# Kernel optimization log

Measured on AMD Instinct MI355X. Metric: run time of the kernel, lower is better.

The kernel has to match this reference:

```python
import jax, jax.numpy as jnp
import numpy as np
import math

EMBED_DIM = 1024
NUM_HEADS = 16
HEAD_DIM = EMBED_DIM // NUM_HEADS
TGT_LEN = 1024
BSZ = 4


def setup_inputs() -> dict:
    key = jax.random.key(0)
    ks = jax.random.split(key, 7)
    # xavier_uniform for in_proj_weight [3E, E]
    limit = math.sqrt(6.0 / (3 * EMBED_DIM + EMBED_DIM))
    in_proj_weight = jax.random.uniform(ks[0], (3 * EMBED_DIM, EMBED_DIM), jnp.float32, -limit, limit)
    in_proj_bias = jnp.zeros((3 * EMBED_DIM,), jnp.float32)
    # out_proj: torch Linear default init (kaiming-uniform-ish); bias zeroed by _reset_parameters
    lim_o = 1.0 / math.sqrt(EMBED_DIM)
    out_proj_weight = jax.random.uniform(ks[1], (EMBED_DIM, EMBED_DIM), jnp.float32, -lim_o, lim_o)
    out_proj_bias = jnp.zeros((EMBED_DIM,), jnp.float32)
    query = jax.random.normal(ks[2], (TGT_LEN, BSZ, EMBED_DIM), jnp.float32)
    key_t = jax.random.normal(ks[3], (TGT_LEN, BSZ, EMBED_DIM), jnp.float32)
    value = jax.random.normal(ks[4], (TGT_LEN, BSZ, EMBED_DIM), jnp.float32)
    return {"query": query, "key": key_t, "value": value,
            "in_proj_weight": in_proj_weight, "in_proj_bias": in_proj_bias,
            "out_proj_weight": out_proj_weight, "out_proj_bias": out_proj_bias}


def reference(query, key, value, in_proj_weight, in_proj_bias, out_proj_weight, out_proj_bias):
    tgt_len, bsz, embed_dim = query.shape
    src_len = key.shape[0]
    w_q, w_k, w_v = jnp.split(in_proj_weight, 3, axis=0)
    b_q, b_k, b_v = jnp.split(in_proj_bias, 3, axis=0)
    q = query @ w_q.T + b_q  # [T, B, E]
    k = key @ w_k.T + b_k    # [S, B, E]
    v = value @ w_v.T + b_v  # [S, B, E]
    # [T, B*H, D] -> [B*H, T, D]
    q = q.reshape(tgt_len, bsz * NUM_HEADS, HEAD_DIM).transpose(1, 0, 2)
    k = k.reshape(src_len, bsz * NUM_HEADS, HEAD_DIM).transpose(1, 0, 2)
    v = v.reshape(src_len, bsz * NUM_HEADS, HEAD_DIM).transpose(1, 0, 2)
    q = q / math.sqrt(embed_dim)  # NOTE: scales by sqrt(embed_dim), not head_dim (faithful)
    attn = jax.nn.sigmoid(jnp.einsum('btd,bsd->bts', q, k))  # [B*H, T, S]
    attn_output = jnp.einsum('bts,bsd->btd', attn, v)         # [B*H, T, D]
    attn_output = attn_output.transpose(1, 0, 2).reshape(tgt_len, bsz, embed_dim)
    attn_output = attn_output @ out_proj_weight.T + out_proj_bias
    return attn_output, attn
```

## Files before the change

kernel.cpp:

```cpp
#include <hip/hip_runtime.h>
#include <stdint.h>

typedef unsigned short u16;
typedef __bf16 bf16x8 __attribute__((ext_vector_type(8)));
typedef float f32x4 __attribute__((ext_vector_type(4)));

__device__ __forceinline__ u16 f2bf(float f) {
  union { float f; uint32_t u; } v; v.f = f;
  uint32_t u = v.u;
  return (u16)((u + 0x7FFFu + ((u >> 16) & 1u)) >> 16);
}

__device__ __forceinline__ void cp16(const void* g, void* lds) {
  __builtin_amdgcn_global_load_lds(
      (const __attribute__((address_space(1))) uint32_t*)(uintptr_t)g,
      (__attribute__((address_space(3))) uint32_t*)(uint32_t)(uintptr_t)lds,
      16, 0, 0);
}

__global__ __launch_bounds__(256) void cvt_kernel(const float* __restrict__ s,
                                                  u16* __restrict__ d, int n4) {
  int i = blockIdx.x * 256 + threadIdx.x;
  if (i >= n4) return;
  float4 f = ((const float4*)s)[i];
  uint2 p;
  p.x = (uint32_t)f2bf(f.x) | ((uint32_t)f2bf(f.y) << 16);
  p.y = (uint32_t)f2bf(f.z) | ((uint32_t)f2bf(f.w) << 16);
  ((uint2*)d)[i] = p;
}

__device__ __forceinline__ void gemm128(const u16* __restrict__ A,
                                        const u16* __restrict__ Bt,
                                        int m0, int n0, int K,
                                        u16* As, u16* Bs, f32x4 acc[4][4]) {
  const int tid = threadIdx.x;
  const int l = tid & 63, w = tid >> 6;
  const int wr = w >> 1, wc = w & 1;
  const int quad = l >> 4, c = l & 15;
  const f32x4 zero = {0.f, 0.f, 0.f, 0.f};
  for (int i = 0; i < 4; ++i)
    for (int j = 0; j < 4; ++j) acc[i][j] = zero;

  for (int k0 = 0; k0 < K; k0 += 64) {
    __syncthreads();
#pragma unroll
    for (int p = 0; p < 4; ++p) {
      int q = p * 256 + tid;
      int row = q >> 3;
      int jj = (q & 7) ^ (row & 7);
      int ldsbase = (p * 256 + (tid & ~63)) * 8;
      cp16(A + (size_t)(m0 + row) * K + k0 + jj * 8, As + ldsbase);
      cp16(Bt + (size_t)(n0 + row) * K + k0 + jj * 8, Bs + ldsbase);
    }
    __syncthreads();
#pragma unroll
    for (int kk = 0; kk < 2; ++kk) {
      bf16x8 af[4], bf[4];
#pragma unroll
      for (int mt = 0; mt < 4; ++mt) {
        int row = wr * 64 + mt * 16 + c;
        af[mt] = *(const bf16x8*)(As + row * 64 + ((((kk << 2) + quad)) ^ (c & 7)) * 8);
      }
#pragma unroll
      for (int nt = 0; nt < 4; ++nt) {
        int row = wc * 64 + nt * 16 + c;
        bf[nt] = *(const bf16x8*)(Bs + row * 64 + ((((kk << 2) + quad)) ^ (c & 7)) * 8);
      }
#pragma unroll
      for (int mt = 0; mt < 4; ++mt)
#pragma unroll
        for (int nt = 0; nt < 4; ++nt)
          acc[mt][nt] = __builtin_amdgcn_mfma_f32_16x16x32_bf16(
              af[mt], bf[nt], acc[mt][nt], 0, 0, 0);
    }
  }
}

__global__ __launch_bounds__(256, 2) void proj_kernel(
    const u16* __restrict__ X, const u16* __restrict__ Win,
    const float* __restrict__ in_bias, u16* __restrict__ Q,
    u16* __restrict__ Kp, u16* __restrict__ Vtmp) {
  __shared__ u16 As[8192], Bs[8192];
  const int which = blockIdx.z;
  const u16* A = X + (size_t)which * (4096 * 1024);
  const u16* Bt = Win + (size_t)which * (1024 * 1024);
  const int m0 = blockIdx.y * 128, n0 = blockIdx.x * 128;
  f32x4 acc[4][4];
  gemm128(A, Bt, m0, n0, 1024, As, Bs, acc);

  u16* dst = (which == 0) ? Q : ((which == 1) ? Kp : Vtmp);
  const float scale = (which == 0) ? 0.03125f : 1.0f;
  const float* bias = in_bias + which * 1024;
  const int l = threadIdx.x & 63, w = threadIdx.x >> 6;
  const int wr = w >> 1, wc = w & 1, quad = l >> 4, c = l & 15;
#pragma unroll
  for (int mt = 0; mt < 4; ++mt)
#pragma unroll
    for (int nt = 0; nt < 4; ++nt) {
      int n = n0 + wc * 64 + nt * 16 + c;
      float bv = bias[n];
      int h = n >> 6, d = n & 63;
#pragma unroll
      for (int r = 0; r < 4; ++r) {
        int m = m0 + wr * 64 + mt * 16 + quad * 4 + r;
        int t = m >> 2, b = m & 3;
        dst[((size_t)((b * 16 + h) * 1024 + t)) * 64 + d] =
            f2bf((acc[mt][nt][r] + bv) * scale);
      }
    }
}

__global__ __launch_bounds__(256, 2) void outproj_kernel(
    const u16* __restrict__ AO, const u16* __restrict__ Wout,
    const float* __restrict__ out_bias, float* __restrict__ out) {
  __shared__ u16 As[8192], Bs[8192];
  const int m0 = blockIdx.y * 128, n0 = blockIdx.x * 128;
  f32x4 acc[4][4];
  gemm128(AO, Wout, m0, n0, 1024, As, Bs, acc);
  const int l = threadIdx.x & 63, w = threadIdx.x >> 6;
  const int wr = w >> 1, wc = w & 1, quad = l >> 4, c = l & 15;
#pragma unroll
  for (int mt = 0; mt < 4; ++mt)
#pragma unroll
    for (int nt = 0; nt < 4; ++nt) {
      int n = n0 + wc * 64 + nt * 16 + c;
      float bv = out_bias[n];
#pragma unroll
      for (int r = 0; r < 4; ++r) {
        int m = m0 + wr * 64 + mt * 16 + quad * 4 + r;
        out[(size_t)m * 1024 + n] = acc[mt][nt][r] + bv;
      }
    }
}

__global__ __launch_bounds__(256) void transpose_v(const u16* __restrict__ Vtmp,
                                                   u16* __restrict__ Vt) {
  __shared__ u16 tile[64 * 72];
  const int bh = blockIdx.y, s0 = blockIdx.x * 64;
  const u16* src = Vtmp + (size_t)bh * 65536;
  u16* dst = Vt + (size_t)bh * 65536;
#pragma unroll
  for (int p = 0; p < 2; ++p) {
    int q = p * 256 + threadIdx.x;
    int sl = q >> 3, dc = q & 7;
    uint4 v = *(const uint4*)(src + (size_t)(s0 + sl) * 64 + dc * 8);
    *(uint4*)&tile[sl * 72 + dc * 8] = v;
  }
  __syncthreads();
#pragma unroll
  for (int p = 0; p < 2; ++p) {
    int q = p * 256 + threadIdx.x;
    int d = q >> 3, sc = q & 7;
    u16 vals[8] __attribute__((aligned(16)));
#pragma unroll
    for (int j = 0; j < 8; ++j) vals[j] = tile[(sc * 8 + j) * 72 + d];
    *(uint4*)(dst + (size_t)d * 1024 + s0 + sc * 8) = *(const uint4*)vals;
  }
}

__global__ __launch_bounds__(256, 2) void attn_kernel(
    const u16* __restrict__ Q, const u16* __restrict__ Kg,
    const u16* __restrict__ Vt, float* __restrict__ attn_out,
    u16* __restrict__ AO) {
  __shared__ u16 Qs[8192];
  __shared__ u16 U[16384];
  __shared__ u16 Vts[8192];
  const int bh = blockIdx.y, t0 = blockIdx.x * 128;
  const int b = bh >> 4, h = bh & 15;
  const int tid = threadIdx.x, l = tid & 63, w = tid >> 6;
  const int quad = l >> 4, c = l & 15;
  const int wr = w >> 1, wc = w & 1;
  const u16* Qbh = Q + (size_t)bh * 65536;
  const u16* Kbh = Kg + (size_t)bh * 65536;
  const u16* Vtbh = Vt + (size_t)bh * 65536;
  float* attnb = attn_out + (size_t)bh * 1048576;

#pragma unroll
  for (int p = 0; p < 4; ++p) {
    int q = p * 256 + tid;
    int row = q >> 3, jj = (q & 7) ^ (row & 7);
    cp16(Qbh + (size_t)(t0 + row) * 64 + jj * 8, Qs + (p * 256 + (tid & ~63)) * 8);
  }

  const f32x4 zero = {0.f, 0.f, 0.f, 0.f};
  f32x4 acc_o[2][4];
  for (int i = 0; i < 2; ++i)
    for (int j = 0; j < 4; ++j) acc_o[i][j] = zero;

  for (int s0 = 0; s0 < 1024; s0 += 128) {
    __syncthreads();
#pragma unroll
    for (int p = 0; p < 4; ++p) {
      int q = p * 256 + tid;
      int row = q >> 3, jj = (q & 7) ^ (row & 7);
      cp16(Kbh + (size_t)(s0 + row) * 64 + jj * 8, U + (p * 256 + (tid & ~63)) * 8);
    }
#pragma unroll
    for (int p = 0; p < 4; ++p) {
      int q = p * 256 + tid;
      int d = q >> 4, sc = q & 15;
      uint4 v = *(const uint4*)(Vtbh + (size_t)d * 1024 + s0 + sc * 8);
      *(uint4*)&Vts[d * 128 + (sc ^ (d & 15)) * 8] = v;
    }
    __syncthreads();

    f32x4 accp[4][4];
    for (int i = 0; i < 4; ++i)
      for (int j = 0; j < 4; ++j) accp[i][j] = zero;
#pragma unroll
    for (int kk = 0; kk < 2; ++kk) {
      bf16x8 af[4], bf[4];
#pragma unroll
      for (int mt = 0; mt < 4; ++mt) {
        int row = wr * 64 + mt * 16 + c;
        af[mt] = *(const bf16x8*)(U + row * 64 + (((kk << 2) + quad) ^ (c & 7)) * 8);
      }
#pragma unroll
      for (int nt = 0; nt < 4; ++nt) {
        int row = wc * 64 + nt * 16 + c;
        bf[nt] = *(const bf16x8*)(Qs + row * 64 + (((kk << 2) + quad) ^ (c & 7)) * 8);
      }
#pragma unroll
      for (int mt = 0; mt < 4; ++mt)
#pragma unroll
        for (int nt = 0; nt < 4; ++nt)
          accp[mt][nt] = __builtin_amdgcn_mfma_f32_16x16x32_bf16(
              af[mt], bf[nt], accp[mt][nt], 0, 0, 0);
    }

#pragma unroll
    for (int mt = 0; mt < 4; ++mt) {
      int sl = wr * 64 + mt * 16 + quad * 4;
#pragma unroll
      for (int nt = 0; nt < 4; ++nt) {
        int t = wc * 64 + nt * 16 + c;
        f32x4 pv;
#pragma unroll
        for (int r = 0; r < 4; ++r)
          pv[r] = 1.0f / (1.0f + __expf(-accp[mt][nt][r]));
        accp[mt][nt] = pv;
        *(f32x4*)(attnb + (size_t)(t0 + t) * 1024 + s0 + sl) = pv;
      }
    }
    __syncthreads();

#pragma unroll
    for (int mt = 0; mt < 4; ++mt) {
      int sbase = wr * 64 + mt * 16 + quad * 4;
      int jw = sbase >> 3, hf = (sbase >> 2) & 1;
#pragma unroll
      for (int nt = 0; nt < 4; ++nt) {
        int t = wc * 64 + nt * 16 + c;
        int jj = jw ^ (t & 15);
        uint2 pk;
        pk.x = (uint32_t)f2bf(accp[mt][nt][0]) | ((uint32_t)f2bf(accp[mt][nt][1]) << 16);
        pk.y = (uint32_t)f2bf(accp[mt][nt][2]) | ((uint32_t)f2bf(accp[mt][nt][3]) << 16);
        *(uint2*)&U[t * 128 + jj * 8 + hf * 4] = pk;
      }
    }
    __syncthreads();

#pragma unroll
    for (int kk = 0; kk < 4; ++kk) {
      bf16x8 ap[2], bv[4];
#pragma unroll
      for (int mt = 0; mt < 2; ++mt) {
        int row = w * 32 + mt * 16 + c;
        ap[mt] = *(const bf16x8*)(U + row * 128 + (((kk << 2) + quad) ^ (row & 15)) * 8);
      }
#pragma unroll
      for (int nt = 0; nt < 4; ++nt) {
        int d = nt * 16 + c;
        bv[nt] = *(const bf16x8*)(Vts + d * 128 + (((kk << 2) + quad) ^ (d & 15)) * 8);
      }
#pragma unroll
      for (int mt = 0; mt < 2; ++mt)
#pragma unroll
        for (int nt = 0; nt < 4; ++nt)
          acc_o[mt][nt] = __builtin_amdgcn_mfma_f32_16x16x32_bf16(
              ap[mt], bv[nt], acc_o[mt][nt], 0, 0, 0);
    }
  }

#pragma unroll
  for (int mt = 0; mt < 2; ++mt)
#pragma unroll
    for (int nt = 0; nt < 4; ++nt) {
      int d = nt * 16 + c;
#pragma unroll
      for (int r = 0; r < 4; ++r) {
        int t = t0 + w * 32 + mt * 16 + quad * 4 + r;
        AO[(size_t)(t * 4 + b) * 1024 + h * 64 + d] = f2bf(acc_o[mt][nt][r]);
      }
    }
}

extern "C" void kernel_launch(void* const* d_in, const int* in_sizes, int n_in,
                              void* d_out, int out_size, void* d_ws, size_t ws_size,
                              hipStream_t stream) {
  const float* query = (const float*)d_in[0];
  const float* key = (const float*)d_in[1];
  const float* value = (const float*)d_in[2];
  const float* in_w = (const float*)d_in[3];
  const float* in_b = (const float*)d_in[4];
  const float* out_w = (const float*)d_in[5];
  const float* out_b = (const float*)d_in[6];
  float* out = (float*)d_out;

  u16* ws = (u16*)d_ws;
  u16* xq = ws;
  u16* win = ws + 12582912;
  u16* wout = ws + 15728640;
  u16* Qp = ws + 16777216;
  u16* Kp = ws + 20971520;
  u16* Vt = ws + 25165824;
  u16* Vtmp = ws + 29360128;
  u16* AO = ws + 33554432;

  cvt_kernel<<<4096, 256, 0, stream>>>(query, xq, 1048576);
  cvt_kernel<<<4096, 256, 0, stream>>>(key, xq + 4194304, 1048576);
  cvt_kernel<<<4096, 256, 0, stream>>>(value, xq + 8388608, 1048576);
  cvt_kernel<<<3072, 256, 0, stream>>>(in_w, win, 786432);
  cvt_kernel<<<1024, 256, 0, stream>>>(out_w, wout, 262144);

  proj_kernel<<<dim3(8, 32, 3), 256, 0, stream>>>(xq, win, in_b, Qp, Kp, Vtmp);
  transpose_v<<<dim3(16, 64), 256, 0, stream>>>(Vtmp, Vt);
  attn_kernel<<<dim3(8, 64), 256, 0, stream>>>(Qp, Kp, Vt, out + 4194304, AO);
  outproj_kernel<<<dim3(8, 32), 256, 0, stream>>>(AO, wout, out_b, out);
}
```

Measured before the change: 485.5 us.

## Fuse conversion launches, give attention a separate P buffer, use nontemporal stores

Merges the five fp32-to-bf16 conversion launches into one kernel. In the attention kernel, K and P get separate LDS buffers (now 80KB of dynamic shared memory), which removes one barrier per tile. The sigmoid now uses hardware exp2 and reciprocal, and the large attention-matrix and output writes use nontemporal stores. The larger LDS footprint may limit blocks per CU, and the approximate rcp/exp2 slightly changes numerics.

```diff
diff --git a/kernel.cpp b/kernel.cpp
--- a/kernel.cpp
+++ b/kernel.cpp
@@ -9,6 +9,11 @@
   union { float f; uint32_t u; } v; v.f = f;
   uint32_t u = v.u;
   return (u16)((u + 0x7FFFu + ((u >> 16) & 1u)) >> 16);
+}
+
+__device__ __forceinline__ float fast_sigmoid(float x) {
+  float e = __builtin_amdgcn_exp2f(x * -1.4426950408889634f);
+  return __builtin_amdgcn_rcpf(1.0f + e);
 }
 
 __device__ __forceinline__ void cp16(const void* g, void* lds) {
@@ -18,15 +23,26 @@
       16, 0, 0);
 }
 
-__global__ __launch_bounds__(256) void cvt_kernel(const float* __restrict__ s,
-                                                  u16* __restrict__ d, int n4) {
+__global__ __launch_bounds__(256) void cvt_all(
+    const float* __restrict__ q, const float* __restrict__ k,
+    const float* __restrict__ v, const float* __restrict__ iw,
+    const float* __restrict__ ow, u16* __restrict__ xq,
+    u16* __restrict__ win, u16* __restrict__ wout) {
   int i = blockIdx.x * 256 + threadIdx.x;
-  if (i >= n4) return;
-  float4 f = ((const float4*)s)[i];
+  const float* s;
+  u16* d;
+  int off;
+  if (i < 2097152) {
+    if (i < 1048576) { s = q; d = xq; off = i; }
+    else { s = k; d = xq + 4194304; off = i - 1048576; }
+  } else if (i < 3145728) { s = v; d = xq + 8388608; off = i - 2097152; }
+  else if (i < 3932160) { s = iw; d = win; off = i - 3145728; }
+  else { s = ow; d = wout; off = i - 3932160; }
+  float4 f = ((const float4*)s)[off];
   uint2 p;
   p.x = (uint32_t)f2bf(f.x) | ((uint32_t)f2bf(f.y) << 16);
   p.y = (uint32_t)f2bf(f.z) | ((uint32_t)f2bf(f.w) << 16);
-  ((uint2*)d)[i] = p;
+  ((uint2*)d)[off] = p;
 }
 
 __device__ __forceinline__ void gemm128(const u16* __restrict__ A,
@@ -128,7 +144,7 @@
 #pragma unroll
       for (int r = 0; r < 4; ++r) {
         int m = m0 + wr * 64 + mt * 16 + quad * 4 + r;
-        out[(size_t)m * 1024 + n] = acc[mt][nt][r] + bv;
+        __builtin_nontemporal_store(acc[mt][nt][r] + bv, &out[(size_t)m * 1024 + n]);
       }
     }
 }
@@ -162,9 +178,11 @@
     const u16* __restrict__ Q, const u16* __restrict__ Kg,
     const u16* __restrict__ Vt, float* __restrict__ attn_out,
     u16* __restrict__ AO) {
-  __shared__ u16 Qs[8192];
-  __shared__ u16 U[16384];
-  __shared__ u16 Vts[8192];
+  extern __shared__ u16 smem[];
+  u16* Qs = smem;
+  u16* Ks = smem + 8192;
+  u16* Vts = smem + 16384;
+  u16* Ps = smem + 24576;
   const int bh = blockIdx.y, t0 = blockIdx.x * 128;
   const int b = bh >> 4, h = bh & 15;
   const int tid = threadIdx.x, l = tid & 63, w = tid >> 6;
@@ -193,7 +211,7 @@
     for (int p = 0; p < 4; ++p) {
       int q = p * 256 + tid;
       int row = q >> 3, jj = (q & 7) ^ (row & 7);
-      cp16(Kbh + (size_t)(s0 + row) * 64 + jj * 8, U + (p * 256 + (tid & ~63)) * 8);
+      cp16(Kbh + (size_t)(s0 + row) * 64 + jj * 8, Ks + (p * 256 + (tid & ~63)) * 8);
     }
 #pragma unroll
     for (int p = 0; p < 4; ++p) {
@@ -213,7 +231,7 @@
 #pragma unroll
       for (int mt = 0; mt < 4; ++mt) {
         int row = wr * 64 + mt * 16 + c;
-        af[mt] = *(const bf16x8*)(U + row * 64 + (((kk << 2) + quad) ^ (c & 7)) * 8);
+        af[mt] = *(const bf16x8*)(Ks + row * 64 + (((kk << 2) + quad) ^ (c & 7)) * 8);
       }
 #pragma unroll
       for (int nt = 0; nt < 4; ++nt) {
@@ -230,35 +248,34 @@
 
 #pragma unroll
     for (int mt = 0; mt < 4; ++mt) {
-      int sl = wr * 64 + mt * 16 + quad * 4;
+      int sbase = wr * 64 + mt * 16 + quad * 4;
+      int jw = sbase >> 3, hf = (sbase >> 2) & 1;
 #pragma unroll
       for (int nt = 0; nt < 4; ++nt) {
         int t = wc * 64 + nt * 16 + c;
         f32x4 pv;
 #pragma unroll
-        for (int r = 0; r < 4; ++r)
-          pv[r] = 1.0f / (1.0f + __expf(-accp[mt][nt][r]));
+        for (int r = 0; r < 4; ++r) pv[r] = fast_sigmoid(accp[mt][nt][r]);
         accp[mt][nt] = pv;
-        *(f32x4*)(attnb + (size_t)(t0 + t) * 1024 + s0 + sl) = pv;
-      }
-    }
-    __syncthreads();
-
-#pragma unroll
-    for (int mt = 0; mt < 4; ++mt) {
-      int sbase = wr * 64 + mt * 16 + quad * 4;
-      int jw = sbase >> 3, hf = (sbase >> 2) & 1;
-#pragma unroll
-      for (int nt = 0; nt < 4; ++nt) {
-        int t = wc * 64 + nt * 16 + c;
         int jj = jw ^ (t & 15);
         uint2 pk;
-        pk.x = (uint32_t)f2bf(accp[mt][nt][0]) | ((uint32_t)f2bf(accp[mt][nt][1]) << 16);
-        pk.y = (uint32_t)f2bf(accp[mt][nt][2]) | ((uint32_t)f2bf(accp[mt][nt][3]) << 16);
-        *(uint2*)&U[t * 128 + jj * 8 + hf * 4] = pk;
-      }
-    }
-    __syncthreads();
+        pk.x = (uint32_t)f2bf(pv[0]) | ((uint32_t)f2bf(pv[1]) << 16);
+        pk.y = (uint32_t)f2bf(pv[2]) | ((uint32_t)f2bf(pv[3]) << 16);
+        *(uint2*)&Ps[t * 128 + jj * 8 + hf * 4] = pk;
+      }
+    }
+    __syncthreads();
+
+#pragma unroll
+    for (int mt = 0; mt < 4; ++mt) {
+      int sl = wr * 64 + mt * 16 + quad * 4;
+#pragma unroll
+      for (int nt = 0; nt < 4; ++nt) {
+        int t = wc * 64 + nt * 16 + c;
+        __builtin_nontemporal_store(
+            accp[mt][nt], (f32x4*)(attnb + (size_t)(t0 + t) * 1024 + s0 + sl));
+      }
+    }
 
 #pragma unroll
     for (int kk = 0; kk < 4; ++kk) {
@@ -266,7 +283,7 @@
 #pragma unroll
       for (int mt = 0; mt < 2; ++mt) {
         int row = w * 32 + mt * 16 + c;
-        ap[mt] = *(const bf16x8*)(U + row * 128 + (((kk << 2) + quad) ^ (row & 15)) * 8);
+        ap[mt] = *(const bf16x8*)(Ps + row * 128 + (((kk << 2) + quad) ^ (row & 15)) * 8);
       }
 #pragma unroll
       for (int nt = 0; nt < 4; ++nt) {
@@ -317,14 +334,12 @@
   u16* Vtmp = ws + 29360128;
   u16* AO = ws + 33554432;
 
-  cvt_kernel<<<4096, 256, 0, stream>>>(query, xq, 1048576);
-  cvt_kernel<<<4096, 256, 0, stream>>>(key, xq + 4194304, 1048576);
-  cvt_kernel<<<4096, 256, 0, stream>>>(value, xq + 8388608, 1048576);
-  cvt_kernel<<<3072, 256, 0, stream>>>(in_w, win, 786432);
-  cvt_kernel<<<1024, 256, 0, stream>>>(out_w, wout, 262144);
-
+  hipFuncSetAttribute((const void*)attn_kernel,
+                      hipFuncAttributeMaxDynamicSharedMemorySize, 81920);
+
+  cvt_all<<<16384, 256, 0, stream>>>(query, key, value, in_w, out_w, xq, win, wout);
   proj_kernel<<<dim3(8, 32, 3), 256, 0, stream>>>(xq, win, in_b, Qp, Kp, Vtmp);
   transpose_v<<<dim3(16, 64), 256, 0, stream>>>(Vtmp, Vt);
-  attn_kernel<<<dim3(8, 64), 256, 0, stream>>>(Qp, Kp, Vt, out + 4194304, AO);
+  attn_kernel<<<dim3(8, 64), 256, 81920, stream>>>(Qp, Kp, Vt, out + 4194304, AO);
   outproj_kernel<<<dim3(8, 32), 256, 0, stream>>>(AO, wout, out_b, out);
 }
```

Result: faster. 470.5 us (-3.1%).
